# Kernel tuning notes

Measured on AMD Instinct MI355X. Metric: run time of the kernel, lower is better.

Reference implementation:

```python
import jax, jax.numpy as jnp
import numpy as np


def conv1x1(x, w, b):
    # x: [B,C,H,W], w: [O,C], b: [O]
    return jnp.einsum('bchw,oc->bohw', x, w) + b[None, :, None, None]


def conv3x3(x, w, b):
    # x: [B,C,H,W], w: [O,C,3,3]
    y = jax.lax.conv_general_dilated(
        x, w, window_strides=(1, 1), padding='SAME',
        dimension_numbers=('NCHW', 'OIHW', 'NCHW'))
    return y + b[None, :, None, None]


def setup_inputs() -> dict:
    key = jax.random.key(0)
    ks = jax.random.split(key, 20)

    def u(k, shape, fan_in):
        # PyTorch Conv2d default init: uniform(-1/sqrt(fan_in), 1/sqrt(fan_in))
        s = 1.0 / np.sqrt(fan_in)
        return jax.random.uniform(k, shape, jnp.float32, -s, s)

    B, H, W = 4, 64, 64
    return {
        'x':   jax.random.normal(ks[0], (B, 3, H, W), jnp.float32),
        # 1x1 stem convs (weights stored as [O,C])
        'w1':  u(ks[1], (64, 3), 3),        'b1':  u(ks[2], (64,), 3),
        'w2':  u(ks[3], (128, 64), 64),     'b2':  u(ks[4], (128,), 64),
        'w3':  u(ks[5], (256, 128), 128),   'b3':  u(ks[6], (256,), 128),
        # 3x3 conv branch (fan_in = 256*9)
        'wb1': u(ks[7], (256, 256, 3, 3), 256 * 9), 'bb1': u(ks[8], (256,), 256 * 9),
        'wb2': u(ks[9], (256, 256, 3, 3), 256 * 9), 'bb2': u(ks[10], (256,), 256 * 9),
        # q/k/v 1x1 convs
        'wq':  u(ks[11], (256, 256), 256),  'bq':  u(ks[12], (256,), 256),
        'wk':  u(ks[13], (256, 256), 256),  'bk':  u(ks[14], (256,), 256),
        'wv':  u(ks[15], (256, 256), 256),  'bv':  u(ks[16], (256,), 256),
        'alpha': jnp.float32(0.5),
        'beta':  jnp.float32(0.5),
    }


def reference(x, w1, b1, w2, b2, w3, b3, wb1, bb1, wb2, bb2,
              wq, bq, wk, bk, wv, bv, alpha, beta):
    x = jax.nn.relu(conv1x1(x, w1, b1))
    x = jax.nn.relu(conv1x1(x, w2, b2))
    x = jax.nn.relu(conv1x1(x, w3, b3))          # [B,256,H,W]
    conv_out = conv3x3(jax.nn.relu(conv3x3(x, wb1, bb1)), wb2, bb2)
    B, C, H, W = x.shape
    q = conv1x1(x, wq, bq).reshape(B, C, -1)     # [B,C,N]
    k = conv1x1(x, wk, bk).reshape(B, C, -1)     # [B,C,N]
    v = conv1x1(x, wv, bv).reshape(B, C, -1)     # [B,C,N]
    # torch: bmm(k^T, q) -> [B,N,N], softmax over last dim
    attn = jax.nn.softmax(jnp.einsum('bcn,bcm->bnm', k, q), axis=-1)
    # torch: bmm(v, attn) -> [B,C,N]
    attn_out = jnp.einsum('bcn,bnm->bcm', v, attn).reshape(B, C, H, W)
    return alpha * conv_out + beta * attn_out
```

## Files before the change

kernel.cpp:

```cpp
#include <hip/hip_runtime.h>
#include <math.h>

#define NPIX 4096
#define CC   256

typedef __attribute__((ext_vector_type(8))) short bf16x8;
typedef __attribute__((ext_vector_type(4))) float f32x4;

__device__ inline unsigned short f2bf(float f) {
    unsigned u = __builtin_bit_cast(unsigned, f);
    u += 0x7FFF + ((u >> 16) & 1);
    return (unsigned short)(u >> 16);
}
__device__ inline float bf2f(unsigned short h) {
    unsigned u = (unsigned)h << 16;
    return __builtin_bit_cast(float, u);
}
__device__ inline void gl_lds16(const unsigned short* g, unsigned short* l) {
    __builtin_amdgcn_global_load_lds(
        (const __attribute__((address_space(1))) void*)g,
        (__attribute__((address_space(3))) void*)l, 16, 0, 0);
}

__global__ __launch_bounds__(256) void prep_kernel(
    const float* __restrict__ w2, const float* __restrict__ w3,
    const float* __restrict__ wq, const float* __restrict__ wk,
    const float* __restrict__ wv, const float* __restrict__ wb1,
    const float* __restrict__ wb2, const float* __restrict__ bq,
    const float* __restrict__ bk,
    unsigned short* w2b, unsigned short* w3b, unsigned short* wqb,
    unsigned short* wkb, unsigned short* wvb,
    unsigned short* wr1, unsigned short* wr2, float* bqk) {
    int i = blockIdx.x * 256 + threadIdx.x;
    if (i < 8192)  w2b[i] = f2bf(w2[i]);
    if (i < 32768) w3b[i] = f2bf(w3[i]);
    if (i < 65536) { wqb[i] = f2bf(wq[i]); wkb[i] = f2bf(wk[i]); wvb[i] = f2bf(wv[i]); }
    if (i < 256)   { bqk[i] = bq[i]; bqk[256 + i] = bk[i]; }
    if (i < 589824) {
        int o = i / 2304; int r = i - o * 2304; int tap = r >> 8; int c = r & 255;
        wr1[i] = f2bf(wb1[(o * 256 + c) * 9 + tap]);
        wr2[i] = f2bf(wb2[(o * 256 + c) * 9 + tap]);
    }
}

__global__ __launch_bounds__(256) void stem1_kernel(
    const float* __restrict__ x, const float* __restrict__ w1,
    const float* __restrict__ b1, unsigned short* __restrict__ h1T) {
    int idx = blockIdx.x * 256 + threadIdx.x;
    int o = idx & 63;
    int p = (idx >> 6) & 4095;
    int b = idx >> 18;
    const float* xb = x + (size_t)b * 3 * NPIX + p;
    float acc = b1[o];
    acc = fmaf(w1[o * 3 + 0], xb[0],        acc);
    acc = fmaf(w1[o * 3 + 1], xb[NPIX],     acc);
    acc = fmaf(w1[o * 3 + 2], xb[2 * NPIX], acc);
    h1T[idx] = f2bf(fmaxf(acc, 0.f));
}

template<int EPI, int KK>
__global__ __launch_bounds__(256) void gemm_fullk(
    const unsigned short* __restrict__ A, long lda, long sA,
    const unsigned short* __restrict__ BT, long ldb, long sB,
    void* __restrict__ Cp, long ldc, long sC,
    const float* __restrict__ bias, float* __restrict__ aux) {
    constexpr int SPR = KK / 8;
    constexpr int RPI = 64 / SPR;
    __shared__ unsigned short As[128 * KK];
    __shared__ unsigned short Bs[128 * KK];
    const int tid  = threadIdx.x;
    const int lane = tid & 63;
    const int wave = tid >> 6;
    const int wr = (wave >> 1) * 64, wc = (wave & 1) * 64;
    const int l15 = lane & 15, lh = lane >> 4;
    const int sl  = lane & (SPR - 1);
    const int rof = lane / SPR;
    const int z = blockIdx.z;
    const unsigned short* Ab = A  + (size_t)z * sA + (size_t)blockIdx.y * 128 * lda;
    const unsigned short* Bb = BT + (size_t)z * sB + (size_t)blockIdx.x * 128 * ldb;

    f32x4 acc[4][4];
    #pragma unroll
    for (int i = 0; i < 4; ++i)
        #pragma unroll
        for (int j = 0; j < 4; ++j) { f32x4 zr = {0.f, 0.f, 0.f, 0.f}; acc[i][j] = zr; }

    #pragma unroll
    for (int i = 0; i < KK / 16; ++i) {
        int r0  = wave * 32 + i * RPI;
        int row = r0 + rof;
        int cs  = (sl ^ (row & (SPR - 1))) * 8;
        gl_lds16(Ab + (size_t)row * lda + cs, &As[r0 * KK]);
        gl_lds16(Bb + (size_t)row * ldb + cs, &Bs[r0 * KK]);
    }
    __syncthreads();

    #pragma unroll
    for (int ks = 0; ks < KK / 32; ++ks) {
        bf16x8 a[4], b[4];
        #pragma unroll
        for (int f = 0; f < 4; ++f) {
            int ra = wr + f * 16 + l15;
            a[f] = *(const bf16x8*)&As[ra * KK + ((((ks << 2) + lh) ^ (ra & (SPR - 1))) << 3)];
            int rb = wc + f * 16 + l15;
            b[f] = *(const bf16x8*)&Bs[rb * KK + ((((ks << 2) + lh) ^ (rb & (SPR - 1))) << 3)];
        }
        #pragma unroll
        for (int i = 0; i < 4; ++i)
            #pragma unroll
            for (int j = 0; j < 4; ++j)
                acc[i][j] = __builtin_amdgcn_mfma_f32_16x16x32_bf16(
                    a[i], b[j], acc[i][j], 0, 0, 0);
    }

    const int row0 = blockIdx.y * 128 + wr;
    const int col0 = blockIdx.x * 128 + wc;
    unsigned short* OUT = (unsigned short*)Cp + (size_t)z * sC;
    #pragma unroll
    for (int i = 0; i < 4; ++i)
        #pragma unroll
        for (int j = 0; j < 4; ++j) {
            int cgl = col0 + j * 16 + l15;
            float bc = (EPI == 1 || EPI == 2) ? bias[cgl] : 0.f;
            float sc = (EPI == 3) ? aux[(size_t)z * 4096 + cgl] : 1.f;
            #pragma unroll
            for (int q = 0; q < 4; ++q) {
                int r = row0 + i * 16 + lh * 4 + q;
                float v = acc[i][j][q];
                if (EPI == 3) v = (v + bias[r]) * sc;
                else v += bc;
                if (EPI == 1) v = fmaxf(v, 0.f);
                OUT[(size_t)r * ldc + cgl] = f2bf(v);
            }
        }
}

template<int EPI>
__global__ __launch_bounds__(512) void gemm256(
    const unsigned short* __restrict__ A, long lda, long sA,
    const unsigned short* __restrict__ BT, long ldb, long sB,
    int Kc, int splits, int nb,
    void* __restrict__ Cp, long ldc, long sC,
    float* __restrict__ aux, float* __restrict__ partial,
    const unsigned short* __restrict__ CV,
    const float* __restrict__ alphaP, const float* __restrict__ betaP,
    int nwgc) {
    __shared__ unsigned short As[2][256 * 64];
    __shared__ unsigned short Bs[2][256 * 64];
    const int orig = blockIdx.x;
    const int wgid = (orig & 7) * nwgc + (orig >> 3);
    int bx, by, sp, z;
    if (EPI == 0) { bx = wgid & 15; by = (wgid >> 4) & 15; z = wgid >> 8; sp = 0; }
    else          { bx = wgid & 15; sp = (wgid >> 4) & (splits - 1); z = wgid / (16 * splits); by = 0; }

    const int tid  = threadIdx.x;
    const int lane = tid & 63;
    const int wave = tid >> 6;
    const int wr = (wave >> 2) * 128;
    const int wc = (wave & 3) * 64;
    const int l15 = lane & 15, lh = lane >> 4;
    const int sl  = lane & 7, rof = lane >> 3;
    const unsigned short* Ab = A  + (size_t)z * sA + (size_t)by * 256 * lda + (size_t)sp * Kc;
    const unsigned short* Bb = BT + (size_t)z * sB + (size_t)bx * 256 * ldb + (size_t)sp * Kc;

    f32x4 acc[8][4];
    #pragma unroll
    for (int i = 0; i < 8; ++i)
        #pragma unroll
        for (int j = 0; j < 4; ++j) { f32x4 zr = {0.f, 0.f, 0.f, 0.f}; acc[i][j] = zr; }

    auto STAGE = [&](int buf, int k0) {
        #pragma unroll
        for (int s = 0; s < 4; ++s) {
            int rb  = wave * 32 + s * 8;
            int row = rb + rof;
            int cs  = (sl ^ (row & 7)) * 8;
            gl_lds16(Ab + (size_t)row * lda + k0 + cs, &As[buf][rb * 64]);
            gl_lds16(Bb + (size_t)row * ldb + k0 + cs, &Bs[buf][rb * 64]);
        }
    };

    STAGE(0, 0);
    const int T = Kc >> 6;
    for (int t = 0; t < T; ++t) {
        const int cur = t & 1;
        if (t + 1 < T) {
            STAGE(cur ^ 1, (t + 1) << 6);
            asm volatile("s_waitcnt vmcnt(8)" ::: "memory");
        } else {
            asm volatile("s_waitcnt vmcnt(0)" ::: "memory");
        }
        __builtin_amdgcn_s_barrier();
        asm volatile("" ::: "memory");
        __builtin_amdgcn_s_setprio(1);
        #pragma unroll
        for (int ks = 0; ks < 2; ++ks) {
            bf16x8 a[8], b[4];
            #pragma unroll
            for (int f = 0; f < 8; ++f) {
                int ra = wr + f * 16 + l15;
                a[f] = *(const bf16x8*)&As[cur][ra * 64 + ((((ks << 2) + lh) ^ (ra & 7)) << 3)];
            }
            #pragma unroll
            for (int f = 0; f < 4; ++f) {
                int rb = wc + f * 16 + l15;
                b[f] = *(const bf16x8*)&Bs[cur][rb * 64 + ((((ks << 2) + lh) ^ (rb & 7)) << 3)];
            }
            #pragma unroll
            for (int i = 0; i < 8; ++i)
                #pragma unroll
                for (int j = 0; j < 4; ++j)
                    acc[i][j] = __builtin_amdgcn_mfma_f32_16x16x32_bf16(
                        a[i], b[j], acc[i][j], 0, 0, 0);
        }
        __builtin_amdgcn_s_setprio(0);
        asm volatile("" ::: "memory");
        __builtin_amdgcn_s_barrier();
    }

    if (EPI == 0) {
        unsigned short* OUT = (unsigned short*)Cp + (size_t)z * sC;
        const int row0 = by * 256 + wr;
        const int col0 = bx * 256 + wc;
        float cs4[4] = {0.f, 0.f, 0.f, 0.f};
        #pragma unroll
        for (int i = 0; i < 8; ++i)
            #pragma unroll
            for (int j = 0; j < 4; ++j) {
                int cgl = col0 + j * 16 + l15;
                #pragma unroll
                for (int q = 0; q < 4; ++q) {
                    int r = row0 + i * 16 + lh * 4 + q;
                    unsigned short h = f2bf(__expf(acc[i][j][q]));
                    OUT[(size_t)r * ldc + cgl] = h;
                    cs4[j] += bf2f(h);
                }
            }
        #pragma unroll
        for (int off = 16; off <= 32; off <<= 1)
            #pragma unroll
            for (int j = 0; j < 4; ++j)
                cs4[j] += __shfl_xor(cs4[j], off);
        if (lh == 0) {
            float* part = aux + (((size_t)z * 16 + by) * 2 + (wave >> 2)) * 4096;
            #pragma unroll
            for (int j = 0; j < 4; ++j)
                part[col0 + j * 16 + l15] = cs4[j];
        }
    } else {
        const int col0 = bx * 256 + wc;
        if (splits == 1) {
            float* OUT = (float*)Cp + (size_t)z * sC;
            const unsigned short* CVb = CV + (size_t)z * sC;
            const float al = alphaP[0], be = betaP[0];
            #pragma unroll
            for (int i = 0; i < 8; ++i)
                #pragma unroll
                for (int j = 0; j < 4; ++j) {
                    int cgl = col0 + j * 16 + l15;
                    #pragma unroll
                    for (int q = 0; q < 4; ++q) {
                        int r = wr + i * 16 + lh * 4 + q;
                        size_t o = (size_t)r * ldc + cgl;
                        OUT[o] = al * bf2f(CVb[o]) + be * acc[i][j][q];
                    }
                }
        } else {
            float* P = partial + ((size_t)sp * nb + z) * ((size_t)256 * 4096);
            #pragma unroll
            for (int i = 0; i < 8; ++i)
                #pragma unroll
                for (int j = 0; j < 4; ++j) {
                    int cgl = col0 + j * 16 + l15;
                    #pragma unroll
                    for (int q = 0; q < 4; ++q) {
                        int r = wr + i * 16 + lh * 4 + q;
                        P[(size_t)r * 4096 + cgl] = acc[i][j][q];
                    }
                }
        }
    }
}

__global__ __launch_bounds__(256) void reduce_kernel(
    const float* __restrict__ partial, const unsigned short* __restrict__ cvb,
    const float* __restrict__ alphaP, const float* __restrict__ betaP,
    float* __restrict__ outp, int splits, long chunk) {
    long idx = ((long)blockIdx.x * 256 + threadIdx.x) * 4;
    if (idx >= chunk) return;
    float4 s = *(const float4*)&partial[idx];
    for (int sp = 1; sp < splits; ++sp) {
        float4 p = *(const float4*)&partial[(size_t)sp * chunk + idx];
        s.x += p.x; s.y += p.y; s.z += p.z; s.w += p.w;
    }
    ushort4 c4 = *(const ushort4*)&cvb[idx];
    const float al = alphaP[0], be = betaP[0];
    float4 r;
    r.x = al * bf2f(c4.x) + be * s.x;
    r.y = al * bf2f(c4.y) + be * s.y;
    r.z = al * bf2f(c4.z) + be * s.z;
    r.w = al * bf2f(c4.w) + be * s.w;
    *(float4*)&outp[idx] = r;
}

__global__ __launch_bounds__(256) void recip_kernel(
    const float* __restrict__ part, float* __restrict__ rcp) {
    int idx = blockIdx.x * 256 + threadIdx.x;
    int z = idx >> 12, n = idx & 4095;
    const float* pb = part + (size_t)z * 32 * 4096 + n;
    float s = 0.f;
    #pragma unroll 8
    for (int t = 0; t < 32; ++t) s += pb[(size_t)t * 4096];
    rcp[idx] = 1.f / s;
}

template<int PIXOUT>
__global__ __launch_bounds__(256) void conv3_v2(
    const unsigned short* __restrict__ X, const unsigned short* __restrict__ Wr,
    const float* __restrict__ bias, void* __restrict__ Outp) {
    __shared__ unsigned short wt[9 * 128 * 40];
    __shared__ unsigned short patch[264 * 40];
    const int tid  = threadIdx.x;
    const int lane = tid & 63;
    const int wave = tid >> 6;
    const int l15 = lane & 15, lh = lane >> 4;
    const int oh = blockIdx.x & 1;
    const int b  = blockIdx.x >> 1;
    const int h0 = blockIdx.y;
    const int wy = (wave >> 1) * 64, wx = (wave & 1) * 64;
    const int obase = PIXOUT ? wx : wy;
    const int pbase = PIXOUT ? wy : wx;
    const unsigned short* Xb  = X + (size_t)b * (NPIX * CC);
    const unsigned short* Wro = Wr + (size_t)oh * 128 * 2304;

    f32x4 acc[4][4];
    #pragma unroll
    for (int i = 0; i < 4; ++i)
        #pragma unroll
        for (int j = 0; j < 4; ++j) { f32x4 zr = {0.f, 0.f, 0.f, 0.f}; acc[i][j] = zr; }

    for (int c0 = 0; c0 < 256; c0 += 32) {
        __syncthreads();
        #pragma unroll
        for (int t = 0; t < 5; ++t) {
            int q = t * 256 + tid;
            if (q < 1056) {
                int slot = q >> 2, cg = (q & 3) * 8;
                int r = slot / 66, w = slot - r * 66;
                int hh = h0 * 2 - 1 + r, ww = w - 1;
                int4 v = make_int4(0, 0, 0, 0);
                if ((unsigned)hh < 64u && (unsigned)ww < 64u)
                    v = *(const int4*)&Xb[(size_t)(hh * 64 + ww) * 256 + c0 + cg];
                *(int4*)&patch[slot * 40 + cg] = v;
            }
        }
        #pragma unroll
        for (int t = 0; t < 18; ++t) {
            int q = t * 256 + tid;
            int o = q / 36, rem = q - o * 36;
            int tap = rem >> 2, cg = (rem & 3) * 8;
            int4 v = *(const int4*)&Wro[(size_t)o * 2304 + tap * 256 + c0 + cg];
            *(int4*)&wt[(tap * 128 + o) * 40 + cg] = v;
        }
        __syncthreads();
        #pragma unroll
        for (int tap = 0; tap < 9; ++tap) {
            const int dy = tap / 3 - 1, dx = tap % 3 - 1;
            bf16x8 wf[4], pf[4];
            #pragma unroll
            for (int f = 0; f < 4; ++f) {
                int o = obase + f * 16 + l15;
                wf[f] = *(const bf16x8*)&wt[(tap * 128 + o) * 40 + lh * 8];
                int p = pbase + f * 16 + l15;
                int slot = ((p >> 6) + dy + 1) * 66 + (p & 63) + dx + 1;
                pf[f] = *(const bf16x8*)&patch[slot * 40 + lh * 8];
            }
            #pragma unroll
            for (int i = 0; i < 4; ++i)
                #pragma unroll
                for (int j = 0; j < 4; ++j) {
                    if (PIXOUT)
                        acc[i][j] = __builtin_amdgcn_mfma_f32_16x16x32_bf16(
                            pf[i], wf[j], acc[i][j], 0, 0, 0);
                    else
                        acc[i][j] = __builtin_amdgcn_mfma_f32_16x16x32_bf16(
                            wf[i], pf[j], acc[i][j], 0, 0, 0);
                }
        }
    }

    const int P0 = h0 * 128;
    if (PIXOUT) {
        unsigned short* O = (unsigned short*)Outp + (size_t)b * (NPIX * CC);
        #pragma unroll
        for (int i = 0; i < 4; ++i)
            #pragma unroll
            for (int j = 0; j < 4; ++j) {
                int o = oh * 128 + obase + j * 16 + l15;
                float bb = bias[o];
                #pragma unroll
                for (int q = 0; q < 4; ++q) {
                    int p = pbase + i * 16 + lh * 4 + q;
                    float v = fmaxf(acc[i][j][q] + bb, 0.f);
                    O[(size_t)(P0 + p) * CC + o] = f2bf(v);
                }
            }
    } else {
        unsigned short* O = (unsigned short*)Outp + (size_t)b * (CC * NPIX);
        #pragma unroll
        for (int i = 0; i < 4; ++i)
            #pragma unroll
            for (int j = 0; j < 4; ++j) {
                #pragma unroll
                for (int q = 0; q < 4; ++q) {
                    int o = oh * 128 + obase + i * 16 + lh * 4 + q;
                    int p = pbase + j * 16 + l15;
                    O[(size_t)o * NPIX + P0 + p] = f2bf(acc[i][j][q] + bias[o]);
                }
            }
    }
}

extern "C" void kernel_launch(void* const* d_in, const int* in_sizes, int n_in,
                              void* d_out, int out_size, void* d_ws, size_t ws_size,
                              hipStream_t stream) {
    const float* x   = (const float*)d_in[0];
    const float* w1  = (const float*)d_in[1];  const float* b1  = (const float*)d_in[2];
    const float* w2  = (const float*)d_in[3];  const float* b2  = (const float*)d_in[4];
    const float* w3  = (const float*)d_in[5];  const float* b3  = (const float*)d_in[6];
    const float* wb1 = (const float*)d_in[7];  const float* bb1 = (const float*)d_in[8];
    const float* wb2 = (const float*)d_in[9];  const float* bb2 = (const float*)d_in[10];
    const float* wq  = (const float*)d_in[11]; const float* bq  = (const float*)d_in[12];
    const float* wk  = (const float*)d_in[13]; const float* bk  = (const float*)d_in[14];
    const float* wv  = (const float*)d_in[15]; const float* bv  = (const float*)d_in[16];
    const float* alpha = (const float*)d_in[17];
    const float* beta  = (const float*)d_in[18];

    const size_t MB = 1 << 20;
    char* wsb = (char*)d_ws;
    unsigned short* x3T = (unsigned short*)(wsb + 0 * MB);
    unsigned short* qkT = (unsigned short*)(wsb + 8 * MB);
    unsigned short* cv  = (unsigned short*)(wsb + 24 * MB);
    unsigned short* t1T = (unsigned short*)(wsb + 32 * MB);
    unsigned short* h1T = (unsigned short*)(wsb + 32 * MB);
    unsigned short* h2T = (unsigned short*)(wsb + 34 * MB);
    unsigned short* vB  = (unsigned short*)(wsb + 40 * MB);
    unsigned short* w2b = (unsigned short*)(wsb + 48 * MB);
    unsigned short* w3b = w2b + 8192;
    unsigned short* wqb = w3b + 32768;
    unsigned short* wkb = wqb + 65536;
    unsigned short* wvb = wkb + 65536;
    unsigned short* wr1 = wvb + 65536;
    unsigned short* wr2 = wr1 + 589824;
    float*          bqk  = (float*)(wsb + 51 * MB);
    float*          part = (float*)(wsb + 52 * MB);
    float*          rcp  = (float*)(wsb + 54 * MB);
    unsigned short* ST   = (unsigned short*)(wsb + 55 * MB);
    float* out = (float*)d_out;
    const long ONEM = (long)CC * NPIX;
    const long SS = 4096L * 4096;

    int nb, splits;
    if      (ws_size >= (size_t)247 * MB) { nb = 4; splits = 4;  }
    else if (ws_size >= (size_t)183 * MB) { nb = 2; splits = 8;  }
    else if (ws_size >= (size_t)151 * MB) { nb = 1; splits = 16; }
    else if (ws_size >= (size_t)119 * MB) { nb = 1; splits = 8;  }
    else if (ws_size >= (size_t)103 * MB) { nb = 1; splits = 4;  }
    else                                  { nb = 1; splits = 1;  }
    float* pvpart = (float*)(wsb + (size_t)(55 + nb * 32) * MB);

    prep_kernel<<<2304, 256, 0, stream>>>(w2, w3, wq, wk, wv, wb1, wb2, bq, bk,
                                          w2b, w3b, wqb, wkb, wvb, wr1, wr2, bqk);
    stem1_kernel<<<4096, 256, 0, stream>>>(x, w1, b1, h1T);

    gemm_fullk<1, 64><<<dim3(1, 32, 4), 256, 0, stream>>>(
        h1T, 64, 4096L * 64, w2b, 64, 0,
        h2T, 128, 4096L * 128, b2, nullptr);
    gemm_fullk<1, 128><<<dim3(2, 32, 4), 256, 0, stream>>>(
        h2T, 128, 4096L * 128, w3b, 128, 0,
        x3T, 256, 4096L * 256, b3, nullptr);
    gemm_fullk<2, 256><<<dim3(4, 32, 4), 256, 0, stream>>>(
        x3T, 256, 4096L * 256, wqb, 256, 0,
        qkT, 512, 4096L * 512, bqk, nullptr);
    conv3_v2<1><<<dim3(8, 32), 256, 0, stream>>>(x3T, wr1, bb1, t1T);
    conv3_v2<0><<<dim3(8, 32), 256, 0, stream>>>(t1T, wr2, bb2, cv);

    for (int b0 = 0; b0 < 4; b0 += nb) {
        int nwgS = 256 * nb;
        gemm256<0><<<nwgS, 512, 0, stream>>>(
            qkT + (size_t)b0 * 4096 * 512, 512, 4096L * 512,
            qkT + (size_t)b0 * 4096 * 512 + 256, 512, 4096L * 512,
            256, 1, nb, ST, 4096, SS,
            part, nullptr, nullptr, nullptr, nullptr, nwgS / 8);
        recip_kernel<<<nb * 16, 256, 0, stream>>>(part, rcp);
        gemm_fullk<3, 256><<<dim3(32, 2, nb), 256, 0, stream>>>(
            wvb, 256, 0,
            x3T + (size_t)b0 * 4096 * 256, 256, 4096L * 256,
            vB, 4096, 256L * 4096, bv, rcp);
        int nwgP = 16 * splits * nb;
        gemm256<4><<<nwgP, 512, 0, stream>>>(
            vB, 4096, 256L * 4096, ST, 4096, SS,
            4096 / splits, splits, nb,
            out + (size_t)b0 * ONEM, 4096, ONEM,
            nullptr, pvpart, cv + (size_t)b0 * ONEM, alpha, beta, nwgP / 8);
        if (splits > 1)
            reduce_kernel<<<nb * 1024, 256, 0, stream>>>(
                pvpart, cv + (size_t)b0 * ONEM, alpha, beta,
                out + (size_t)b0 * ONEM, splits, (long)nb * ONEM);
    }
}
```

Before: 253.8 us.

## Split GEMM k-tile into four barrier-fenced MFMA phases with interleaved prefetch

```diff
diff --git a/kernel.cpp b/kernel.cpp
--- a/kernel.cpp
+++ b/kernel.cpp
@@ -135,6 +135,90 @@
         }
 }
 
+#define PH_ENTER                                            \
+    asm volatile("" ::: "memory");                          \
+    __builtin_amdgcn_s_barrier();                           \
+    asm volatile("s_waitcnt lgkmcnt(0)" ::: "memory");      \
+    __builtin_amdgcn_sched_barrier(0);                      \
+    __builtin_amdgcn_s_setprio(1);
+#define PH_EXIT                                             \
+    __builtin_amdgcn_s_setprio(0);                          \
+    asm volatile("" ::: "memory");                          \
+    __builtin_amdgcn_s_barrier();
+
+#define DO_TILE(CURA, CURB, NXTA, NXTB, KT)                                    \
+{                                                                              \
+    const int kn_ = (KT) + 1;                                                  \
+    bf16x8 aL[4][2], aH[4][2], b01[2][2], b23[2][2];                           \
+                                 \
+    _Pragma("unroll") for (int f = 0; f < 4; ++f) {                            \
+        const unsigned short* rp = &(CURA)[(wr + f * 16 + l15) * 64];          \
+        aL[f][0] = *(const bf16x8*)&rp[sa0];                                   \
+        aL[f][1] = *(const bf16x8*)&rp[sa1];                                   \
+    }                                                                          \
+    _Pragma("unroll") for (int f = 0; f < 2; ++f) {                            \
+        const unsigned short* rp = &(CURB)[(wc + f * 16 + l15) * 64];          \
+        b01[f][0] = *(const bf16x8*)&rp[sa0];                                  \
+        b01[f][1] = *(const bf16x8*)&rp[sa1];                                  \
+    }                                                                          \
+    if (kn_ < T) {                                                             \
+        _Pragma("unroll") for (int s = 0; s < 4; ++s) {                        \
+            int rb_ = wave * 32 + s * 8;                                       \
+            gl_lds16(Ab + (size_t)(rb_ + rof) * lda + (kn_ << 6) + csw,        \
+                     &(NXTA)[rb_ * 64]);                                       \
+        }                                                                      \
+    }                                                                          \
+    PH_ENTER;                                                                  \
+    _Pragma("unroll") for (int i = 0; i < 4; ++i)                              \
+        _Pragma("unroll") for (int j = 0; j < 2; ++j)                          \
+            _Pragma("unroll") for (int ks = 0; ks < 2; ++ks)                   \
+                acc[i][j] = __builtin_amdgcn_mfma_f32_16x16x32_bf16(           \
+                    aL[i][ks], b01[j][ks], acc[i][j], 0, 0, 0);                \
+    PH_EXIT;                                                                   \
+                                      \
+    _Pragma("unroll") for (int f = 0; f < 2; ++f) {                            \
+        const unsigned short* rp = &(CURB)[(wc + 32 + f * 16 + l15) * 64];     \
+        b23[f][0] = *(const bf16x8*)&rp[sa0];                                  \
+        b23[f][1] = *(const bf16x8*)&rp[sa1];                                  \
+    }                                                                          \
+    if (kn_ < T) {                                                             \
+        _Pragma("unroll") for (int s = 0; s < 4; ++s) {                        \
+            int rb_ = wave * 32 + s * 8;                                       \
+            gl_lds16(Bb + (size_t)(rb_ + rof) * ldb + (kn_ << 6) + csw,        \
+                     &(NXTB)[rb_ * 64]);                                       \
+        }                                                                      \
+    }                                                                          \
+    PH_ENTER;                                                                  \
+    _Pragma("unroll") for (int i = 0; i < 4; ++i)                              \
+        _Pragma("unroll") for (int j = 0; j < 2; ++j)                          \
+            _Pragma("unroll") for (int ks = 0; ks < 2; ++ks)                   \
+                acc[i][j + 2] = __builtin_amdgcn_mfma_f32_16x16x32_bf16(       \
+                    aL[i][ks], b23[j][ks], acc[i][j + 2], 0, 0, 0);            \
+    PH_EXIT;                                                                   \
+                                                    \
+    _Pragma("unroll") for (int f = 0; f < 4; ++f) {                            \
+        const unsigned short* rp = &(CURA)[(wr + 64 + f * 16 + l15) * 64];     \
+        aH[f][0] = *(const bf16x8*)&rp[sa0];                                   \
+        aH[f][1] = *(const bf16x8*)&rp[sa1];                                   \
+    }                                                                          \
+    PH_ENTER;                                                                  \
+    _Pragma("unroll") for (int i = 0; i < 4; ++i)                              \
+        _Pragma("unroll") for (int j = 0; j < 2; ++j)                          \
+            _Pragma("unroll") for (int ks = 0; ks < 2; ++ks)                   \
+                acc[i + 4][j + 2] = __builtin_amdgcn_mfma_f32_16x16x32_bf16(   \
+                    aH[i][ks], b23[j][ks], acc[i + 4][j + 2], 0, 0, 0);        \
+    PH_EXIT;                                                                   \
+                                             \
+    asm volatile("s_waitcnt vmcnt(0)" ::: "memory");                           \
+    PH_ENTER;                                                                  \
+    _Pragma("unroll") for (int i = 0; i < 4; ++i)                              \
+        _Pragma("unroll") for (int j = 0; j < 2; ++j)                          \
+            _Pragma("unroll") for (int ks = 0; ks < 2; ++ks)                   \
+                acc[i + 4][j] = __builtin_amdgcn_mfma_f32_16x16x32_bf16(       \
+                    aH[i][ks], b01[j][ks], acc[i + 4][j], 0, 0, 0);            \
+    PH_EXIT;                                                                   \
+}
+
 template<int EPI>
 __global__ __launch_bounds__(512) void gemm256(
     const unsigned short* __restrict__ A, long lda, long sA,
@@ -145,8 +229,8 @@
     const unsigned short* __restrict__ CV,
     const float* __restrict__ alphaP, const float* __restrict__ betaP,
     int nwgc) {
-    __shared__ unsigned short As[2][256 * 64];
-    __shared__ unsigned short Bs[2][256 * 64];
+    __shared__ unsigned short As0[256 * 64], As1[256 * 64];
+    __shared__ unsigned short Bs0[256 * 64], Bs1[256 * 64];
     const int orig = blockIdx.x;
     const int wgid = (orig & 7) * nwgc + (orig >> 3);
     int bx, by, sp, z;
@@ -160,6 +244,9 @@
     const int wc = (wave & 3) * 64;
     const int l15 = lane & 15, lh = lane >> 4;
     const int sl  = lane & 7, rof = lane >> 3;
+    const int csw = (sl ^ rof) * 8;
+    const int sa0 = ((lh ^ (l15 & 7)) << 3);
+    const int sa1 = (((4 + lh) ^ (l15 & 7)) << 3);
     const unsigned short* Ab = A  + (size_t)z * sA + (size_t)by * 256 * lda + (size_t)sp * Kc;
     const unsigned short* Bb = BT + (size_t)z * sB + (size_t)bx * 256 * ldb + (size_t)sp * Kc;
 
@@ -169,53 +256,19 @@
         #pragma unroll
         for (int j = 0; j < 4; ++j) { f32x4 zr = {0.f, 0.f, 0.f, 0.f}; acc[i][j] = zr; }
 
-    auto STAGE = [&](int buf, int k0) {
-        #pragma unroll
-        for (int s = 0; s < 4; ++s) {
-            int rb  = wave * 32 + s * 8;
-            int row = rb + rof;
-            int cs  = (sl ^ (row & 7)) * 8;
-            gl_lds16(Ab + (size_t)row * lda + k0 + cs, &As[buf][rb * 64]);
-            gl_lds16(Bb + (size_t)row * ldb + k0 + cs, &Bs[buf][rb * 64]);
-        }
-    };
-
-    STAGE(0, 0);
     const int T = Kc >> 6;
-    for (int t = 0; t < T; ++t) {
-        const int cur = t & 1;
-        if (t + 1 < T) {
-            STAGE(cur ^ 1, (t + 1) << 6);
-            asm volatile("s_waitcnt vmcnt(8)" ::: "memory");
-        } else {
-            asm volatile("s_waitcnt vmcnt(0)" ::: "memory");
-        }
-        __builtin_amdgcn_s_barrier();
-        asm volatile("" ::: "memory");
-        __builtin_amdgcn_s_setprio(1);
-        #pragma unroll
-        for (int ks = 0; ks < 2; ++ks) {
-            bf16x8 a[8], b[4];
-            #pragma unroll
-            for (int f = 0; f < 8; ++f) {
-                int ra = wr + f * 16 + l15;
-                a[f] = *(const bf16x8*)&As[cur][ra * 64 + ((((ks << 2) + lh) ^ (ra & 7)) << 3)];
-            }
-            #pragma unroll
-            for (int f = 0; f < 4; ++f) {
-                int rb = wc + f * 16 + l15;
-                b[f] = *(const bf16x8*)&Bs[cur][rb * 64 + ((((ks << 2) + lh) ^ (rb & 7)) << 3)];
-            }
-            #pragma unroll
-            for (int i = 0; i < 8; ++i)
-                #pragma unroll
-                for (int j = 0; j < 4; ++j)
-                    acc[i][j] = __builtin_amdgcn_mfma_f32_16x16x32_bf16(
-                        a[i], b[j], acc[i][j], 0, 0, 0);
-        }
-        __builtin_amdgcn_s_setprio(0);
-        asm volatile("" ::: "memory");
-        __builtin_amdgcn_s_barrier();
+    #pragma unroll
+    for (int s = 0; s < 4; ++s) {
+        int rb = wave * 32 + s * 8;
+        gl_lds16(Ab + (size_t)(rb + rof) * lda + csw, &As0[rb * 64]);
+        gl_lds16(Bb + (size_t)(rb + rof) * ldb + csw, &Bs0[rb * 64]);
+    }
+    asm volatile("s_waitcnt vmcnt(0)" ::: "memory");
+    __builtin_amdgcn_s_barrier();
+
+    for (int kt = 0; kt < T; kt += 2) {
+        DO_TILE(As0, Bs0, As1, Bs1, kt);
+        DO_TILE(As1, Bs1, As0, Bs0, kt + 1);
     }
 
     if (EPI == 0) {
```

Measured after the change: 245.4 us. -3.3%, faster.

## Halve gemm256 K-tile, store split-K partials in bf16, double split count

Applied to the files above, without the earlier changes.

```diff
diff --git a/kernel.cpp b/kernel.cpp
--- a/kernel.cpp
+++ b/kernel.cpp
@@ -16,7 +16,7 @@
     unsigned u = (unsigned)h << 16;
     return __builtin_bit_cast(float, u);
 }
-__device__ inline void gl_lds16(const unsigned short* g, unsigned short* l) {
+__device__ inline void gl_lds16(const void* g, void* l) {
     __builtin_amdgcn_global_load_lds(
         (const __attribute__((address_space(1))) void*)g,
         (__attribute__((address_space(3))) void*)l, 16, 0, 0);
@@ -136,22 +136,22 @@
 }
 
 template<int EPI>
-__global__ __launch_bounds__(512) void gemm256(
+__global__ __launch_bounds__(512, 4) void gemm256(
     const unsigned short* __restrict__ A, long lda, long sA,
     const unsigned short* __restrict__ BT, long ldb, long sB,
     int Kc, int splits, int nb,
     void* __restrict__ Cp, long ldc, long sC,
-    float* __restrict__ aux, float* __restrict__ partial,
+    float* __restrict__ aux, unsigned short* __restrict__ partial,
     const unsigned short* __restrict__ CV,
     const float* __restrict__ alphaP, const float* __restrict__ betaP,
     int nwgc) {
-    __shared__ unsigned short As[2][256 * 64];
-    __shared__ unsigned short Bs[2][256 * 64];
+    __shared__ unsigned short As[2][256 * 32];
+    __shared__ unsigned short Bs[2][256 * 32];
     const int orig = blockIdx.x;
     const int wgid = (orig & 7) * nwgc + (orig >> 3);
     int bx, by, sp, z;
     if (EPI == 0) { bx = wgid & 15; by = (wgid >> 4) & 15; z = wgid >> 8; sp = 0; }
-    else          { bx = wgid & 15; sp = (wgid >> 4) & (splits - 1); z = wgid / (16 * splits); by = 0; }
+    else          { bx = wgid & 15; sp = (wgid >> 4) % splits; z = wgid / (16 * splits); by = 0; }
 
     const int tid  = threadIdx.x;
     const int lane = tid & 63;
@@ -159,7 +159,7 @@
     const int wr = (wave >> 2) * 128;
     const int wc = (wave & 3) * 64;
     const int l15 = lane & 15, lh = lane >> 4;
-    const int sl  = lane & 7, rof = lane >> 3;
+    const int srow = lane >> 2, sslot = lane & 3;
     const unsigned short* Ab = A  + (size_t)z * sA + (size_t)by * 256 * lda + (size_t)sp * Kc;
     const unsigned short* Bb = BT + (size_t)z * sB + (size_t)bx * 256 * ldb + (size_t)sp * Kc;
 
@@ -171,40 +171,39 @@
 
     auto STAGE = [&](int buf, int k0) {
         #pragma unroll
-        for (int s = 0; s < 4; ++s) {
-            int rb  = wave * 32 + s * 8;
-            int row = rb + rof;
-            int cs  = (sl ^ (row & 7)) * 8;
-            gl_lds16(Ab + (size_t)row * lda + k0 + cs, &As[buf][rb * 64]);
-            gl_lds16(Bb + (size_t)row * ldb + k0 + cs, &Bs[buf][rb * 64]);
+        for (int s = 0; s < 2; ++s) {
+            int rb  = wave * 32 + s * 16;
+            int row = rb + srow;
+            int cs  = (sslot ^ ((row >> 1) & 3)) * 8;
+            gl_lds16(Ab + (size_t)row * lda + k0 + cs, &As[buf][rb * 32]);
+            gl_lds16(Bb + (size_t)row * ldb + k0 + cs, &Bs[buf][rb * 32]);
         }
     };
 
     STAGE(0, 0);
-    const int T = Kc >> 6;
+    const int T = Kc >> 5;
     for (int t = 0; t < T; ++t) {
         const int cur = t & 1;
         if (t + 1 < T) {
-            STAGE(cur ^ 1, (t + 1) << 6);
-            asm volatile("s_waitcnt vmcnt(8)" ::: "memory");
+            STAGE(cur ^ 1, (t + 1) << 5);
+            asm volatile("s_waitcnt vmcnt(4)" ::: "memory");
         } else {
             asm volatile("s_waitcnt vmcnt(0)" ::: "memory");
         }
         __builtin_amdgcn_s_barrier();
         asm volatile("" ::: "memory");
         __builtin_amdgcn_s_setprio(1);
-        #pragma unroll
-        for (int ks = 0; ks < 2; ++ks) {
+        {
             bf16x8 a[8], b[4];
             #pragma unroll
             for (int f = 0; f < 8; ++f) {
                 int ra = wr + f * 16 + l15;
-                a[f] = *(const bf16x8*)&As[cur][ra * 64 + ((((ks << 2) + lh) ^ (ra & 7)) << 3)];
+                a[f] = *(const bf16x8*)&As[cur][ra * 32 + ((lh ^ ((ra >> 1) & 3)) << 3)];
             }
             #pragma unroll
             for (int f = 0; f < 4; ++f) {
                 int rb = wc + f * 16 + l15;
-                b[f] = *(const bf16x8*)&Bs[cur][rb * 64 + ((((ks << 2) + lh) ^ (rb & 7)) << 3)];
+                b[f] = *(const bf16x8*)&Bs[cur][rb * 32 + ((lh ^ ((rb >> 1) & 3)) << 3)];
             }
             #pragma unroll
             for (int i = 0; i < 8; ++i)
@@ -266,7 +265,7 @@
                     }
                 }
         } else {
-            float* P = partial + ((size_t)sp * nb + z) * ((size_t)256 * 4096);
+            unsigned short* P = partial + ((size_t)sp * nb + z) * ((size_t)256 * 4096);
             #pragma unroll
             for (int i = 0; i < 8; ++i)
                 #pragma unroll
@@ -275,7 +274,7 @@
                     #pragma unroll
                     for (int q = 0; q < 4; ++q) {
                         int r = wr + i * 16 + lh * 4 + q;
-                        P[(size_t)r * 4096 + cgl] = acc[i][j][q];
+                        P[(size_t)r * 4096 + cgl] = f2bf(acc[i][j][q]);
                     }
                 }
         }
@@ -283,23 +282,23 @@
 }
 
 __global__ __launch_bounds__(256) void reduce_kernel(
-    const float* __restrict__ partial, const unsigned short* __restrict__ cvb,
+    const unsigned short* __restrict__ partial, const unsigned short* __restrict__ cvb,
     const float* __restrict__ alphaP, const float* __restrict__ betaP,
     float* __restrict__ outp, int splits, long chunk) {
     long idx = ((long)blockIdx.x * 256 + threadIdx.x) * 4;
     if (idx >= chunk) return;
-    float4 s = *(const float4*)&partial[idx];
-    for (int sp = 1; sp < splits; ++sp) {
-        float4 p = *(const float4*)&partial[(size_t)sp * chunk + idx];
-        s.x += p.x; s.y += p.y; s.z += p.z; s.w += p.w;
+    float s0 = 0.f, s1 = 0.f, s2 = 0.f, s3 = 0.f;
+    for (int sp = 0; sp < splits; ++sp) {
+        ushort4 p = *(const ushort4*)&partial[(size_t)sp * chunk + idx];
+        s0 += bf2f(p.x); s1 += bf2f(p.y); s2 += bf2f(p.z); s3 += bf2f(p.w);
     }
     ushort4 c4 = *(const ushort4*)&cvb[idx];
     const float al = alphaP[0], be = betaP[0];
     float4 r;
-    r.x = al * bf2f(c4.x) + be * s.x;
-    r.y = al * bf2f(c4.y) + be * s.y;
-    r.z = al * bf2f(c4.z) + be * s.z;
-    r.w = al * bf2f(c4.w) + be * s.w;
+    r.x = al * bf2f(c4.x) + be * s0;
+    r.y = al * bf2f(c4.y) + be * s1;
+    r.z = al * bf2f(c4.z) + be * s2;
+    r.w = al * bf2f(c4.w) + be * s3;
     *(float4*)&outp[idx] = r;
 }
 
@@ -461,13 +460,11 @@
     const long SS = 4096L * 4096;
 
     int nb, splits;
-    if      (ws_size >= (size_t)247 * MB) { nb = 4; splits = 4;  }
-    else if (ws_size >= (size_t)183 * MB) { nb = 2; splits = 8;  }
-    else if (ws_size >= (size_t)151 * MB) { nb = 1; splits = 16; }
-    else if (ws_size >= (size_t)119 * MB) { nb = 1; splits = 8;  }
-    else if (ws_size >= (size_t)103 * MB) { nb = 1; splits = 4;  }
+    if      (ws_size >= (size_t)247 * MB) { nb = 4; splits = 8;  }
+    else if (ws_size >= (size_t)183 * MB) { nb = 2; splits = 16; }
+    else if (ws_size >= (size_t)119 * MB) { nb = 1; splits = 16; }
     else                                  { nb = 1; splits = 1;  }
-    float* pvpart = (float*)(wsb + (size_t)(55 + nb * 32) * MB);
+    unsigned short* pvpart = (unsigned short*)(wsb + (size_t)(55 + nb * 32) * MB);
 
     prep_kernel<<<2304, 256, 0, stream>>>(w2, w3, wq, wk, wv, wb1, wb2, bq, bk,
                                           w2b, w3b, wqb, wkb, wvb, wr1, wr2, bqk);
```

Measured after the change: 669.7 us. 2.64x slower.
